# Kernel tuning notes

Measured on AMD Instinct MI355X. Metric: run time of the kernel, lower is better.

## Reference

```python
import jax, jax.numpy as jnp
import numpy as np

HS, FF, NH = 1024, 4096, 16
HD = HS // NH
EPS = 1e-5

def _ln(x, g, b):
    m = jnp.mean(x, axis=-1, keepdims=True)
    v = jnp.mean((x - m) ** 2, axis=-1, keepdims=True)
    return (x - m) * jax.lax.rsqrt(v + EPS) * g + b

def setup_inputs() -> dict:
    key = jax.random.key(0)
    ks = jax.random.split(key, 12)
    s = 1.0 / np.sqrt(HS)
    si = 1.0 / np.sqrt(FF)
    d = {
        "hidden_states": jax.random.normal(ks[0], (2, 2048, HS), dtype=jnp.float32),
        "attention_mask": jnp.zeros((2, 1, 1, 2048), dtype=jnp.float32),
        "Wq": jax.random.uniform(ks[1], (HS, HS), minval=-s, maxval=s),
        "bq": jnp.zeros((HS,), jnp.float32),
        "Wk": jax.random.uniform(ks[2], (HS, HS), minval=-s, maxval=s),
        "bk": jnp.zeros((HS,), jnp.float32),
        "Wv": jax.random.uniform(ks[3], (HS, HS), minval=-s, maxval=s),
        "bv": jnp.zeros((HS,), jnp.float32),
        "Wo": jax.random.uniform(ks[4], (HS, HS), minval=-s, maxval=s),
        "bo": jnp.zeros((HS,), jnp.float32),
        "W1": jax.random.uniform(ks[5], (HS, FF), minval=-s, maxval=s),
        "b1": jnp.zeros((FF,), jnp.float32),
        "W2": jax.random.uniform(ks[6], (FF, HS), minval=-si, maxval=si),
        "b2": jnp.zeros((HS,), jnp.float32),
        "ln1_g": jnp.ones((HS,), jnp.float32),
        "ln1_b": jnp.zeros((HS,), jnp.float32),
        "ln2_g": jnp.ones((HS,), jnp.float32),
        "ln2_b": jnp.zeros((HS,), jnp.float32),
    }
    return d

def reference(hidden_states, attention_mask, Wq, bq, Wk, bk, Wv, bv, Wo, bo,
              W1, b1, W2, b2, ln1_g, ln1_b, ln2_g, ln2_b):
    bs, S, _ = hidden_states.shape
    x = hidden_states
    # self-attention (dropout is identity in eval)
    q = (x @ Wq + bq).reshape(bs, S, NH, HD).transpose(0, 2, 1, 3)
    k = (x @ Wk + bk).reshape(bs, S, NH, HD).transpose(0, 2, 1, 3)
    v = (x @ Wv + bv).reshape(bs, S, NH, HD).transpose(0, 2, 1, 3)
    scores = jnp.einsum("bhqd,bhkd->bhqk", q, k) / np.sqrt(HD) + attention_mask
    probs = jax.nn.softmax(scores, axis=-1)
    attn = jnp.einsum("bhqk,bhkd->bhqd", probs, v)
    attn = attn.transpose(0, 2, 1, 3).reshape(bs, S, HS)
    mha = attn @ Wo + bo
    h = _ln(x + mha, ln1_g, ln1_b)
    # FFN
    ff = jax.nn.relu(h @ W1 + b1) @ W2 + b2
    return _ln(h + ff, ln2_g, ln2_b)
```

## Files before the change

kernel.cpp:

```cpp
#include <hip/hip_runtime.h>
#include <hip/hip_bf16.h>

#define HS   1024
#define FF   4096
#define NH   16
#define HD   64
#define SEQ  2048
#define BSZ  2
#define MROWS (BSZ * SEQ)
#define EPS  1e-5f
#define QKV_STRIDE (3 * HS)

typedef float f32x4  __attribute__((ext_vector_type(4)));
typedef short bf16x8 __attribute__((ext_vector_type(8)));

__device__ __forceinline__ unsigned short f2bf(float x) {
  unsigned int u = __float_as_uint(x);
  u += 0x7fffu + ((u >> 16) & 1u);
  return (unsigned short)(u >> 16);
}

__device__ __forceinline__ unsigned int pkbf(float a, float b) {
  union { __hip_bfloat162 h; unsigned int u; } x;
  x.h = __float22bfloat162_rn(float2{a, b});
  return x.u;
}

__device__ __forceinline__ void async16(const ushort* g, ushort* lds) {
  __builtin_amdgcn_global_load_lds(
      (const __attribute__((address_space(1))) unsigned int*)g,
      (__attribute__((address_space(3))) unsigned int*)lds, 16, 0, 0);
}

template <int TBM, int TBN, bool RELU, bool OUT_BF16, bool PARTIAL>
__global__ __launch_bounds__(256) void gemm_bf16_kernel(
    const ushort* __restrict__ A, const ushort* __restrict__ Bt,
    const float* __restrict__ bias, void* __restrict__ Cout,
    int M, int N, int K, int kLen, size_t zstride)
{
  constexpr int MI = TBM / 32;
  constexpr int NJ = TBN / 32;
  __shared__ ushort As[TBM * 64];
  __shared__ ushort Bs[TBN * 64];

  const int tid = threadIdx.x;
  const int wv = tid >> 6, ln = tid & 63;
  const int bn = blockIdx.x, bm = blockIdx.y;

  const int lr = ln & 15;
  const int lg = ln >> 4;
  const int mrow_base = (wv >> 1) * (TBM / 2);
  const int ncol_base = (wv & 1) * (TBN / 2);

  f32x4 acc[MI][NJ];
#pragma unroll
  for (int i = 0; i < MI; ++i)
#pragma unroll
    for (int j = 0; j < NJ; ++j) acc[i][j] = (f32x4){0.f, 0.f, 0.f, 0.f};

  const int rr = ln >> 3, cc = ln & 7;
  const int kBeg = blockIdx.z * kLen, kEnd = kBeg + kLen;

  for (int k0 = kBeg; k0 < kEnd; k0 += 64) {
    __syncthreads();
#pragma unroll
    for (int t = 0; t < TBM / 32; ++t) {
      const int R = wv * (TBM / 4) + t * 8 + rr;
      const int c = cc ^ (R & 7);
      async16(A + (size_t)(bm * TBM + R) * K + k0 + c * 8,
              &As[(size_t)(wv * (TBM / 4) + t * 8) * 64]);
    }
#pragma unroll
    for (int t = 0; t < TBN / 32; ++t) {
      const int R = wv * (TBN / 4) + t * 8 + rr;
      const int c = cc ^ (R & 7);
      async16(Bt + (size_t)(bn * TBN + R) * K + k0 + c * 8,
              &Bs[(size_t)(wv * (TBN / 4) + t * 8) * 64]);
    }
    __syncthreads();

#pragma unroll
    for (int s = 0; s < 2; ++s) {
      bf16x8 a[MI], b[NJ];
#pragma unroll
      for (int i = 0; i < MI; ++i) {
        const int m = mrow_base + i * 16 + lr;
        a[i] = *(const bf16x8*)&As[(size_t)m * 64 + (((s * 4 + lg) ^ (m & 7)) * 8)];
      }
#pragma unroll
      for (int j = 0; j < NJ; ++j) {
        const int n = ncol_base + j * 16 + lr;
        b[j] = *(const bf16x8*)&Bs[(size_t)n * 64 + (((s * 4 + lg) ^ (n & 7)) * 8)];
      }
#pragma unroll
      for (int i = 0; i < MI; ++i)
#pragma unroll
        for (int j = 0; j < NJ; ++j)
          acc[i][j] = __builtin_amdgcn_mfma_f32_16x16x32_bf16(a[i], b[j], acc[i][j], 0, 0, 0);
    }
  }

  const int gm0 = bm * TBM + mrow_base;
  const int gn0 = bn * TBN + ncol_base;

  if (PARTIAL) {
    float* Cp = (float*)Cout + (size_t)blockIdx.z * zstride;
#pragma unroll
    for (int i = 0; i < MI; ++i)
#pragma unroll
      for (int r = 0; r < 4; ++r) {
        const size_t row = (size_t)(gm0 + i * 16 + lg * 4 + r);
#pragma unroll
        for (int j = 0; j < NJ; ++j)
          Cp[row * N + gn0 + j * 16 + lr] = acc[i][j][r];
      }
  } else {
    float bs4[NJ];
#pragma unroll
    for (int j = 0; j < NJ; ++j) bs4[j] = bias[gn0 + j * 16 + lr];
    float* Cf = (float*)Cout;
    ushort* Cb = (ushort*)Cout;
#pragma unroll
    for (int i = 0; i < MI; ++i) {
#pragma unroll
      for (int r = 0; r < 4; ++r) {
        const size_t row = (size_t)(gm0 + i * 16 + lg * 4 + r);
#pragma unroll
        for (int j = 0; j < NJ; ++j) {
          float val = acc[i][j][r] + bs4[j];
          if (RELU) val = fmaxf(val, 0.f);
          const size_t idx = row * N + gn0 + j * 16 + lr;
          if (OUT_BF16) Cb[idx] = f2bf(val);
          else          Cf[idx] = val;
        }
      }
    }
  }
}

__device__ __forceinline__ void transpose_tile(
    const float* __restrict__ W, ushort* __restrict__ Wt,
    int K, int N, int n0, int k0, int tid, ushort (*T)[72])
{
#pragma unroll
  for (int t = 0; t < 4; ++t) {
    const int r = t * 16 + (tid >> 4);
    const int c = (tid & 15) * 4;
    const float4 w = *(const float4*)&W[(size_t)(k0 + r) * N + n0 + c];
    T[c + 0][r] = f2bf(w.x); T[c + 1][r] = f2bf(w.y);
    T[c + 2][r] = f2bf(w.z); T[c + 3][r] = f2bf(w.w);
  }
  __syncthreads();
#pragma unroll
  for (int t = 0; t < 4; ++t) {
    const int n = t * 16 + (tid >> 4);
    const int kc = (tid & 15) * 4;
    ushort4 o;
    o.x = T[n][kc]; o.y = T[n][kc + 1]; o.z = T[n][kc + 2]; o.w = T[n][kc + 3];
    *(ushort4*)&Wt[(size_t)(n0 + n) * K + k0 + kc] = o;
  }
}

__global__ __launch_bounds__(256) void prep_kernel(
    const float* __restrict__ Wq, const float* __restrict__ Wk,
    const float* __restrict__ Wv, const float* __restrict__ Wo,
    const float* __restrict__ W1, const float* __restrict__ W2,
    const float* __restrict__ bq, const float* __restrict__ bk,
    const float* __restrict__ bv, const float* __restrict__ x,
    ushort* __restrict__ Wqkvt, ushort* __restrict__ Wot,
    ushort* __restrict__ W1t, ushort* __restrict__ W2t,
    float* __restrict__ bqkv, ushort* __restrict__ xb)
{
  __shared__ ushort T[64][72];
  const int b = blockIdx.x, tid = threadIdx.x;
  const size_t M1 = 1024 * 1024;
  if (b < 1024) {
    const int w = b >> 8, l = b & 255;
    const int n0 = (l & 15) * 64, k0 = (l >> 4) * 64;
    const float* src = (w == 0) ? Wq : (w == 1) ? Wk : (w == 2) ? Wv : Wo;
    ushort* dst = (w < 3) ? (Wqkvt + (size_t)w * M1) : Wot;
    transpose_tile(src, dst, HS, HS, n0, k0, tid, T);
  } else if (b < 2048) {
    const int l = b - 1024;
    transpose_tile(W1, W1t, HS, FF, (l & 63) * 64, (l >> 6) * 64, tid, T);
  } else if (b < 3072) {
    const int l = b - 2048;
    transpose_tile(W2, W2t, FF, HS, (l & 15) * 64, (l >> 4) * 64, tid, T);
  } else if (b < 5120) {
    const size_t base = (size_t)(b - 3072) * 2048 + tid * 8;
    const float4 v0 = *(const float4*)&x[base];
    const float4 v1 = *(const float4*)&x[base + 4];
    ushort4 o0, o1;
    o0.x = f2bf(v0.x); o0.y = f2bf(v0.y); o0.z = f2bf(v0.z); o0.w = f2bf(v0.w);
    o1.x = f2bf(v1.x); o1.y = f2bf(v1.y); o1.z = f2bf(v1.z); o1.w = f2bf(v1.w);
    *(ushort4*)&xb[base] = o0;
    *(ushort4*)&xb[base + 4] = o1;
  } else {
#pragma unroll
    for (int t = 0; t < 12; ++t) {
      const int i = t * 256 + tid;
      bqkv[i] = (i < HS) ? bq[i] : (i < 2 * HS) ? bk[i - HS] : bv[i - 2 * HS];
    }
  }
}

__global__ __launch_bounds__(256) void vtrans_kernel(
    const ushort* __restrict__ vb, ushort* __restrict__ VTg, int stride)
{
  __shared__ ushort T[64][68];
  const int tid = threadIdx.x;
  const int s0 = blockIdx.x * 64;
  const int bh = blockIdx.y;
  const int b = bh >> 4, h = bh & 15;
#pragma unroll
  for (int t = 0; t < 4; ++t) {
    const int rr = t * 16 + (tid >> 4);
    const int c4 = (tid & 15) * 4;
    const ushort4 w = *(const ushort4*)&vb[(size_t)(b * SEQ + s0 + rr) * stride + h * 64 + c4];
    T[c4 + 0][rr] = w.x; T[c4 + 1][rr] = w.y;
    T[c4 + 2][rr] = w.z; T[c4 + 3][rr] = w.w;
  }
  __syncthreads();
#pragma unroll
  for (int t = 0; t < 4; ++t) {
    const int d = t * 16 + (tid >> 4);
    const int k4 = (tid & 15) * 4;
    ushort4 o;
    o.x = T[d][k4]; o.y = T[d][k4 + 1]; o.z = T[d][k4 + 2]; o.w = T[d][k4 + 3];
    *(ushort4*)&VTg[((size_t)bh * 64 + d) * SEQ + s0 + k4] = o;
  }
}

__global__ __launch_bounds__(512, 4) void attention_mfma_kernel(
    const ushort* __restrict__ Qb, const ushort* __restrict__ Kb,
    const ushort* __restrict__ VTg, const float* __restrict__ mask,
    ushort* __restrict__ O)
{
  __shared__ ushort smem[32768];
  ushort* Ks  = smem;
  ushort* VTs = smem + 8192;
  ushort* Ps  = smem + 16384;

  const int tid = threadIdx.x;
  const int wv = tid >> 6, ln = tid & 63;
  const int c = ln & 15, g = ln >> 4;
  const int qt = blockIdx.x, hh = blockIdx.y, b = blockIdx.z;
  const int bh = b * NH + hh;
  const size_t row0 = (size_t)b * SEQ + (size_t)qt * 128;
  const int ch = hh * HD;
  const int wq0 = wv * 16;

  bf16x8 qf[2];
#pragma unroll
  for (int s = 0; s < 2; ++s)
    qf[s] = *(const bf16x8*)&Qb[(row0 + wq0 + c) * QKV_STRIDE + ch + s * 32 + g * 8];

  f32x4 ao[4];
#pragma unroll
  for (int i = 0; i < 4; ++i) ao[i] = (f32x4){0, 0, 0, 0};
  float l_r = 0.f;

  ushort* Pw = Ps + wv * 2048;
  const int rr = ln >> 3, cc = ln & 7;
  const int r4 = ln >> 4, sc = ln & 15;

  for (int kb = 0; kb < SEQ / 128; ++kb) {
    __syncthreads();
    const size_t krow0 = (size_t)b * SEQ + (size_t)kb * 128;
#pragma unroll
    for (int t = 0; t < 2; ++t) {
      const int r = wv * 16 + t * 8 + rr;
      async16(Kb + (krow0 + r) * QKV_STRIDE + ch + ((cc ^ (r & 7)) * 8),
              &Ks[(size_t)(wv * 16 + t * 8) * 64]);
    }
#pragma unroll
    for (int t = 0; t < 2; ++t) {
      const int d = wv * 8 + t * 4 + r4;
      const int srcc = (sc & 8) | ((sc & 7) ^ (d & 7));
      async16(VTg + ((size_t)bh * 64 + d) * SEQ + kb * 128 + srcc * 8,
              &VTs[(size_t)(wv * 8 + t * 4) * 128]);
    }
    __syncthreads();

    f32x4 as_[8];
#pragma unroll
    for (int i = 0; i < 8; ++i) as_[i] = (f32x4){0, 0, 0, 0};
#pragma unroll
    for (int s = 0; s < 2; ++s) {
#pragma unroll
      for (int mt = 0; mt < 8; ++mt) {
        const int key = mt * 16 + c;
        const bf16x8 kf = *(const bf16x8*)&Ks[(size_t)key * 64 + (((s * 4 + g) ^ (key & 7)) * 8)];
        as_[mt] = __builtin_amdgcn_mfma_f32_16x16x32_bf16(kf, qf[s], as_[mt], 0, 0, 0);
      }
    }

    float lsum = 0.f;
#pragma unroll
    for (int mt = 0; mt < 8; ++mt) {
      const float4 mk = *(const float4*)&mask[(size_t)b * SEQ + kb * 128 + mt * 16 + g * 4];
#pragma unroll
      for (int r = 0; r < 4; ++r) {
        const float mkv = (r == 0) ? mk.x : (r == 1) ? mk.y : (r == 2) ? mk.z : mk.w;
        const float p = __expf(fminf(as_[mt][r] * 0.125f + mkv, 60.f));
        as_[mt][r] = p;
        lsum += p;
      }
    }
    l_r += lsum;

#pragma unroll
    for (int mt = 0; mt < 8; ++mt) {
      const int kc = 2 * mt + (g >> 1);
      const int slot = (kc & 8) | ((kc & 7) ^ (c & 7));
      const int base = c * 128 + slot * 8 + 4 * (g & 1);
      uint2 w;
      w.x = pkbf(as_[mt][0], as_[mt][1]);
      w.y = pkbf(as_[mt][2], as_[mt][3]);
      *(uint2*)&Pw[base] = w;
    }

#pragma unroll
    for (int s = 0; s < 4; ++s) {
      const int k = s * 4 + g;
      const int pslot = (k & 8) | ((k & 7) ^ (c & 7));
      const bf16x8 pf = *(const bf16x8*)&Pw[(size_t)c * 128 + pslot * 8];
#pragma unroll
      for (int mt = 0; mt < 4; ++mt) {
        const int d = mt * 16 + c;
        const int vslot = (k & 8) | ((k & 7) ^ (d & 7));
        const bf16x8 vf = *(const bf16x8*)&VTs[(size_t)d * 128 + vslot * 8];
        ao[mt] = __builtin_amdgcn_mfma_f32_16x16x32_bf16(vf, pf, ao[mt], 0, 0, 0);
      }
    }
  }

  l_r += __shfl_xor(l_r, 16, 64);
  l_r += __shfl_xor(l_r, 32, 64);

  __syncthreads();
  ushort* OL = smem;
  {
    const float inv = 1.f / l_r;
    const int q = wq0 + c;
#pragma unroll
    for (int mt = 0; mt < 4; ++mt) {
      const int d = mt * 16 + g * 4;
      uint2 w;
      w.x = pkbf(ao[mt][0] * inv, ao[mt][1] * inv);
      w.y = pkbf(ao[mt][2] * inv, ao[mt][3] * inv);
      *(uint2*)&OL[q * 72 + d] = w;
    }
  }
  __syncthreads();
#pragma unroll
  for (int it = 0; it < 2; ++it) {
    const int unit = it * 512 + tid;
    const int q = unit >> 3, sg = unit & 7;
    const uint4 w = *(const uint4*)&OL[q * 72 + sg * 8];
    *(uint4*)&O[(row0 + q) * HS + ch + sg * 8] = w;
  }
}

template <bool EMIT16>
__global__ __launch_bounds__(256) void add_ln_red_kernel(
    const float* __restrict__ P0, const float* __restrict__ P1,
    const float* __restrict__ bias, const float* __restrict__ X,
    const float* __restrict__ g, const float* __restrict__ b,
    float* __restrict__ out, ushort* __restrict__ outb)
{
  const int row = blockIdx.x;
  const int tid = threadIdx.x;
  const size_t base = (size_t)row * HS + tid * 4;
  const float4 p0 = *(const float4*)&P0[base];
  const float4 p1 = *(const float4*)&P1[base];
  const float4 bi = *(const float4*)&bias[tid * 4];
  const float4 xv = *(const float4*)&X[base];
  float4 v;
  v.x = xv.x + p0.x + p1.x + bi.x;
  v.y = xv.y + p0.y + p1.y + bi.y;
  v.z = xv.z + p0.z + p1.z + bi.z;
  v.w = xv.w + p0.w + p1.w + bi.w;
  float s1 = v.x + v.y + v.z + v.w;
  float s2 = v.x * v.x + v.y * v.y + v.z * v.z + v.w * v.w;
#pragma unroll
  for (int off = 32; off > 0; off >>= 1) {
    s1 += __shfl_down(s1, off, 64);
    s2 += __shfl_down(s2, off, 64);
  }
  __shared__ float red[8];
  __shared__ float stat[2];
  const int wid = tid >> 6;
  if ((tid & 63) == 0) { red[wid] = s1; red[4 + wid] = s2; }
  __syncthreads();
  if (tid == 0) {
    const float t1 = red[0] + red[1] + red[2] + red[3];
    const float t2 = red[4] + red[5] + red[6] + red[7];
    const float mean = t1 * (1.f / HS);
    const float var = t2 * (1.f / HS) - mean * mean;
    stat[0] = mean;
    stat[1] = rsqrtf(var + EPS);
  }
  __syncthreads();
  const float mean = stat[0], rstd = stat[1];
  const float4 gv = *(const float4*)&g[tid * 4];
  const float4 bv = *(const float4*)&b[tid * 4];
  float4 r;
  r.x = (v.x - mean) * rstd * gv.x + bv.x;
  r.y = (v.y - mean) * rstd * gv.y + bv.y;
  r.z = (v.z - mean) * rstd * gv.z + bv.z;
  r.w = (v.w - mean) * rstd * gv.w + bv.w;
  *(float4*)&out[base] = r;
  if (EMIT16) {
    ushort4 o;
    o.x = f2bf(r.x); o.y = f2bf(r.y); o.z = f2bf(r.z); o.w = f2bf(r.w);
    *(ushort4*)&outb[base] = o;
  }
}

extern "C" void kernel_launch(void* const* d_in, const int* in_sizes, int n_in,
                              void* d_out, int out_size, void* d_ws, size_t ws_size,
                              hipStream_t stream)
{
  const float* x    = (const float*)d_in[0];
  const float* mask = (const float*)d_in[1];
  const float* Wq   = (const float*)d_in[2];  const float* bq  = (const float*)d_in[3];
  const float* Wk   = (const float*)d_in[4];  const float* bk  = (const float*)d_in[5];
  const float* Wv   = (const float*)d_in[6];  const float* bv  = (const float*)d_in[7];
  const float* Wo   = (const float*)d_in[8];  const float* bo  = (const float*)d_in[9];
  const float* W1   = (const float*)d_in[10]; const float* b1  = (const float*)d_in[11];
  const float* W2   = (const float*)d_in[12]; const float* b2  = (const float*)d_in[13];
  const float* g1   = (const float*)d_in[14]; const float* be1 = (const float*)d_in[15];
  const float* g2   = (const float*)d_in[16]; const float* be2 = (const float*)d_in[17];
  float* out = (float*)d_out;

  ushort* wsu = (ushort*)d_ws;
  const size_t M1 = 1024 * 1024;

  ushort* Wqkvt = wsu;
  ushort* Wot   = wsu + 3 * M1;
  ushort* W1t   = wsu + 4 * M1;
  ushort* W2t   = wsu + 8 * M1;
  float*  bqkv  = (float*)(wsu + 12 * M1);
  ushort* xb    = wsu + 13 * M1;
  ushort* qkvb  = wsu + 17 * M1;
  ushort* VTg   = wsu + 29 * M1;
  ushort* attnb = wsu + 33 * M1;
  float*  woP   = (float*)(wsu + 13 * M1);
  float*  h     = (float*)(wsu + 29 * M1);
  ushort* hb    = wsu + 37 * M1;
  ushort* ff1o  = wsu + 13 * M1;
  float*  ff2P0 = (float*)wsu;
  float*  ff2P1 = (float*)(wsu + 39 * M1);

  const dim3 blk(256);
  const size_t SLAB = (size_t)MROWS * HS;

  prep_kernel<<<dim3(5121), blk, 0, stream>>>(
      Wq, Wk, Wv, Wo, W1, W2, bq, bk, bv, x,
      Wqkvt, Wot, W1t, W2t, bqkv, xb);

  gemm_bf16_kernel<128, 128, false, true, false><<<dim3(24, 32), blk, 0, stream>>>(
      xb, Wqkvt, bqkv, qkvb, MROWS, 3 * HS, HS, HS, 0);

  vtrans_kernel<<<dim3(SEQ / 64, BSZ * NH), blk, 0, stream>>>(qkvb + 2 * HS, VTg, QKV_STRIDE);

  attention_mfma_kernel<<<dim3(SEQ / 128, NH, BSZ), dim3(512), 0, stream>>>(
      qkvb, qkvb + HS, VTg, mask, attnb);

  gemm_bf16_kernel<64, 128, false, false, true><<<dim3(8, 64, 2), blk, 0, stream>>>(
      attnb, Wot, nullptr, woP, MROWS, HS, HS, HS / 2, SLAB);
  add_ln_red_kernel<true><<<dim3(MROWS), blk, 0, stream>>>(
      woP, woP + SLAB, bo, x, g1, be1, h, hb);

  gemm_bf16_kernel<128, 128, true, true, false><<<dim3(32, 32), blk, 0, stream>>>(
      hb, W1t, b1, ff1o, MROWS, FF, HS, HS, 0);
  gemm_bf16_kernel<128, 128, false, false, true><<<dim3(8, 32, 2), blk, 0, stream>>>(
      ff1o, W2t, nullptr, ff2P0, MROWS, HS, FF, FF / 2, (size_t)(ff2P1 - ff2P0));
  add_ln_red_kernel<false><<<dim3(MROWS), blk, 0, stream>>>(
      ff2P0, ff2P1, b2, h, g2, be2, out, nullptr);
}
```

Measured before the change: 395.1 us.

## Give each attention wave two query tiles and halve block size to 256 threads

The attention kernel now runs 4 waves per block instead of 8, and each wave handles 32 query rows as two 16-row tiles. Each K and V fragment read from shared memory feeds two MFMAs, which halves LDS traffic per MFMA. Each thread issues twice as many async loads per key block. The cost is more accumulator registers per wave and fewer waves per block to hide latency, which the launch bounds change to (256,2) accounts for.

```diff
diff --git a/kernel.cpp b/kernel.cpp
--- a/kernel.cpp
+++ b/kernel.cpp
@@ -231,7 +231,7 @@
   }
 }
 
-__global__ __launch_bounds__(512, 4) void attention_mfma_kernel(
+__global__ __launch_bounds__(256, 2) void attention_mfma_kernel(
     const ushort* __restrict__ Qb, const ushort* __restrict__ Kb,
     const ushort* __restrict__ VTg, const float* __restrict__ mask,
     ushort* __restrict__ O)
@@ -248,19 +248,21 @@
   const int bh = b * NH + hh;
   const size_t row0 = (size_t)b * SEQ + (size_t)qt * 128;
   const int ch = hh * HD;
-  const int wq0 = wv * 16;
-
-  bf16x8 qf[2];
-#pragma unroll
-  for (int s = 0; s < 2; ++s)
-    qf[s] = *(const bf16x8*)&Qb[(row0 + wq0 + c) * QKV_STRIDE + ch + s * 32 + g * 8];
-
-  f32x4 ao[4];
-#pragma unroll
-  for (int i = 0; i < 4; ++i) ao[i] = (f32x4){0, 0, 0, 0};
-  float l_r = 0.f;
-
-  ushort* Pw = Ps + wv * 2048;
+  const int wq0 = wv * 32;
+
+  bf16x8 qf[2][2];
+#pragma unroll
+  for (int nt = 0; nt < 2; ++nt)
+#pragma unroll
+    for (int s = 0; s < 2; ++s)
+      qf[nt][s] = *(const bf16x8*)&Qb[(row0 + wq0 + nt * 16 + c) * QKV_STRIDE + ch + s * 32 + g * 8];
+
+  f32x4 ao[4][2];
+#pragma unroll
+  for (int i = 0; i < 4; ++i) { ao[i][0] = (f32x4){0,0,0,0}; ao[i][1] = (f32x4){0,0,0,0}; }
+  float l_r[2] = {0.f, 0.f};
+
+  ushort* Pw = Ps + wv * 4096;
   const int rr = ln >> 3, cc = ln & 7;
   const int r4 = ln >> 4, sc = ln & 15;
 
@@ -268,94 +270,112 @@
     __syncthreads();
     const size_t krow0 = (size_t)b * SEQ + (size_t)kb * 128;
 #pragma unroll
-    for (int t = 0; t < 2; ++t) {
-      const int r = wv * 16 + t * 8 + rr;
+    for (int t = 0; t < 4; ++t) {
+      const int r = wv * 32 + t * 8 + rr;
       async16(Kb + (krow0 + r) * QKV_STRIDE + ch + ((cc ^ (r & 7)) * 8),
-              &Ks[(size_t)(wv * 16 + t * 8) * 64]);
-    }
-#pragma unroll
-    for (int t = 0; t < 2; ++t) {
-      const int d = wv * 8 + t * 4 + r4;
+              &Ks[(size_t)(wv * 32 + t * 8) * 64]);
+    }
+#pragma unroll
+    for (int t = 0; t < 4; ++t) {
+      const int d = wv * 16 + t * 4 + r4;
       const int srcc = (sc & 8) | ((sc & 7) ^ (d & 7));
       async16(VTg + ((size_t)bh * 64 + d) * SEQ + kb * 128 + srcc * 8,
-              &VTs[(size_t)(wv * 8 + t * 4) * 128]);
+              &VTs[(size_t)(wv * 16 + t * 4) * 128]);
     }
     __syncthreads();
 
-    f32x4 as_[8];
-#pragma unroll
-    for (int i = 0; i < 8; ++i) as_[i] = (f32x4){0, 0, 0, 0};
+    f32x4 as_[8][2];
+#pragma unroll
+    for (int i = 0; i < 8; ++i) { as_[i][0] = (f32x4){0,0,0,0}; as_[i][1] = (f32x4){0,0,0,0}; }
 #pragma unroll
     for (int s = 0; s < 2; ++s) {
 #pragma unroll
       for (int mt = 0; mt < 8; ++mt) {
         const int key = mt * 16 + c;
         const bf16x8 kf = *(const bf16x8*)&Ks[(size_t)key * 64 + (((s * 4 + g) ^ (key & 7)) * 8)];
-        as_[mt] = __builtin_amdgcn_mfma_f32_16x16x32_bf16(kf, qf[s], as_[mt], 0, 0, 0);
-      }
-    }
-
-    float lsum = 0.f;
+#pragma unroll
+        for (int nt = 0; nt < 2; ++nt)
+          as_[mt][nt] = __builtin_amdgcn_mfma_f32_16x16x32_bf16(kf, qf[nt][s], as_[mt][nt], 0, 0, 0);
+      }
+    }
+
 #pragma unroll
     for (int mt = 0; mt < 8; ++mt) {
       const float4 mk = *(const float4*)&mask[(size_t)b * SEQ + kb * 128 + mt * 16 + g * 4];
-#pragma unroll
-      for (int r = 0; r < 4; ++r) {
-        const float mkv = (r == 0) ? mk.x : (r == 1) ? mk.y : (r == 2) ? mk.z : mk.w;
-        const float p = __expf(fminf(as_[mt][r] * 0.125f + mkv, 60.f));
-        as_[mt][r] = p;
-        lsum += p;
-      }
-    }
-    l_r += lsum;
+      const float mka[4] = {mk.x, mk.y, mk.z, mk.w};
+#pragma unroll
+      for (int nt = 0; nt < 2; ++nt) {
+#pragma unroll
+        for (int r = 0; r < 4; ++r) {
+          const float p = __expf(fminf(as_[mt][nt][r] * 0.125f + mka[r], 60.f));
+          as_[mt][nt][r] = p;
+          l_r[nt] += p;
+        }
+      }
+    }
 
 #pragma unroll
     for (int mt = 0; mt < 8; ++mt) {
       const int kc = 2 * mt + (g >> 1);
       const int slot = (kc & 8) | ((kc & 7) ^ (c & 7));
-      const int base = c * 128 + slot * 8 + 4 * (g & 1);
-      uint2 w;
-      w.x = pkbf(as_[mt][0], as_[mt][1]);
-      w.y = pkbf(as_[mt][2], as_[mt][3]);
-      *(uint2*)&Pw[base] = w;
+#pragma unroll
+      for (int nt = 0; nt < 2; ++nt) {
+        const int q = nt * 16 + c;
+        const int base = q * 128 + slot * 8 + 4 * (g & 1);
+        uint2 w;
+        w.x = pkbf(as_[mt][nt][0], as_[mt][nt][1]);
+        w.y = pkbf(as_[mt][nt][2], as_[mt][nt][3]);
+        *(uint2*)&Pw[base] = w;
+      }
     }
 
 #pragma unroll
     for (int s = 0; s < 4; ++s) {
       const int k = s * 4 + g;
-      const int pslot = (k & 8) | ((k & 7) ^ (c & 7));
-      const bf16x8 pf = *(const bf16x8*)&Pw[(size_t)c * 128 + pslot * 8];
+      bf16x8 pf[2];
+#pragma unroll
+      for (int nt = 0; nt < 2; ++nt) {
+        const int q = nt * 16 + c;
+        const int pslot = (k & 8) | ((k & 7) ^ (q & 7));
+        pf[nt] = *(const bf16x8*)&Pw[(size_t)q * 128 + pslot * 8];
+      }
 #pragma unroll
       for (int mt = 0; mt < 4; ++mt) {
         const int d = mt * 16 + c;
         const int vslot = (k & 8) | ((k & 7) ^ (d & 7));
         const bf16x8 vf = *(const bf16x8*)&VTs[(size_t)d * 128 + vslot * 8];
-        ao[mt] = __builtin_amdgcn_mfma_f32_16x16x32_bf16(vf, pf, ao[mt], 0, 0, 0);
-      }
-    }
-  }
-
-  l_r += __shfl_xor(l_r, 16, 64);
-  l_r += __shfl_xor(l_r, 32, 64);
+#pragma unroll
+        for (int nt = 0; nt < 2; ++nt)
+          ao[mt][nt] = __builtin_amdgcn_mfma_f32_16x16x32_bf16(vf, pf[nt], ao[mt][nt], 0, 0, 0);
+      }
+    }
+  }
+
+#pragma unroll
+  for (int nt = 0; nt < 2; ++nt) {
+    l_r[nt] += __shfl_xor(l_r[nt], 16, 64);
+    l_r[nt] += __shfl_xor(l_r[nt], 32, 64);
+  }
 
   __syncthreads();
   ushort* OL = smem;
-  {
-    const float inv = 1.f / l_r;
-    const int q = wq0 + c;
+#pragma unroll
+  for (int nt = 0; nt < 2; ++nt) {
+    const float inv = 1.f / l_r[nt];
+    const int q = wq0 + nt * 16 + c;
 #pragma unroll
     for (int mt = 0; mt < 4; ++mt) {
       const int d = mt * 16 + g * 4;
       uint2 w;
-      w.x = pkbf(ao[mt][0] * inv, ao[mt][1] * inv);
-      w.y = pkbf(ao[mt][2] * inv, ao[mt][3] * inv);
+      w.x = pkbf(ao[mt][nt][0] * inv, ao[mt][nt][1] * inv);
+      w.y = pkbf(ao[mt][nt][2] * inv, ao[mt][nt][3] * inv);
       *(uint2*)&OL[q * 72 + d] = w;
     }
   }
   __syncthreads();
 #pragma unroll
-  for (int it = 0; it < 2; ++it) {
-    const int unit = it * 512 + tid;
+  for (int it = 0; it < 4; ++it) {
+    const int unit = it * 256 + tid;
     const int q = unit >> 3, sg = unit & 7;
     const uint4 w = *(const uint4*)&OL[q * 72 + sg * 8];
     *(uint4*)&O[(row0 + q) * HS + ch + sg * 8] = w;
@@ -465,7 +485,7 @@
 
   vtrans_kernel<<<dim3(SEQ / 64, BSZ * NH), blk, 0, stream>>>(qkvb + 2 * HS, VTg, QKV_STRIDE);
 
-  attention_mfma_kernel<<<dim3(SEQ / 128, NH, BSZ), dim3(512), 0, stream>>>(
+  attention_mfma_kernel<<<dim3(SEQ / 128, NH, BSZ), blk, 0, stream>>>(
       qkvb, qkvb + HS, VTg, mask, attnb);
 
   gemm_bf16_kernel<64, 128, false, false, true><<<dim3(8, 64, 2), blk, 0, stream>>>(
```

New measurement: 377.9 us. 1.05x faster.
